# Optimization experiments

Hardware: AMD Instinct MI355X
Metric: run time of the kernel (lower is better)

Reference implementation:

```python
import jax, jax.numpy as jnp
import numpy as np

N_NODES = 50000
N_HOPS = 4
N_EDGES = 800000
NFEAT = 512
HIDDEN = 512
NCLASS = 128
ATT_HID = 64


def setup_inputs() -> dict:
    key = jax.random.key(0)
    ks = jax.random.split(key, 12)
    s = lambda *sh: 1.0 / np.sqrt(sh[0])
    inp = {}
    inp['x'] = jax.random.normal(ks[0], (N_NODES, NFEAT), dtype=jnp.float32)
    inp['W1'] = jax.random.normal(ks[1], (NFEAT, HIDDEN), dtype=jnp.float32) * s(NFEAT)
    inp['W2'] = jax.random.normal(ks[2], (HIDDEN, NCLASS), dtype=jnp.float32) * s(HIDDEN)
    inp['b2'] = jax.random.normal(ks[3], (NCLASS,), dtype=jnp.float32) * 0.01
    inp['Wg'] = jax.random.normal(ks[4], (NCLASS, NCLASS), dtype=jnp.float32) * s(NCLASS)
    inp['Wa'] = jax.random.normal(ks[5], (2 * NCLASS, ATT_HID), dtype=jnp.float32) * s(2 * NCLASS)
    inp['ba'] = jax.random.normal(ks[6], (ATT_HID,), dtype=jnp.float32) * 0.01
    inp['va'] = jax.random.normal(ks[7], (ATT_HID,), dtype=jnp.float32) * s(ATT_HID)
    inp['adj_values'] = jax.random.uniform(ks[8], (N_HOPS, N_EDGES), dtype=jnp.float32)
    inp['adj_indices'] = jax.random.randint(ks[9], (N_HOPS, 2, N_EDGES), 0, N_NODES, dtype=jnp.int32)
    inp['idx'] = jnp.arange(N_NODES, dtype=jnp.int32)
    return inp


def reference(x, W1, W2, b2, Wg, Wa, ba, va, adj_values, adj_indices, idx):
    # x: [N, nfeat] -> relu(linear1) -> linear2 : [N, C]
    z = jax.nn.relu(x @ W1) @ W2 + b2  # [N, C]
    anchor = z[idx]                    # [Na, C]
    na = idx.shape[0]
    n_hops = adj_indices.shape[0]
    embs = [anchor]
    for h in range(n_hops):  # fixed small structural loop over hops
        rows = adj_indices[h, 0]  # destination anchor row per edge
        cols = adj_indices[h, 1]  # source node per edge
        # sparse matmul: agg[r] = sum_e v_e * z[cols_e]  (LayerConvol)
        agg = jax.ops.segment_sum(adj_values[h][:, None] * z[cols], rows, num_segments=na)
        embs.append(agg @ Wg)  # [Na, C]
    seq = jnp.stack(embs, axis=1)  # [Na, H+1, C]
    # AttenMlp: additive attention of anchor query over hop embeddings
    q = jnp.broadcast_to(anchor[:, None, :], seq.shape)       # [Na, H+1, C]
    feat = jnp.concatenate([q, seq], axis=-1)                 # [Na, H+1, 2C]
    scores = jnp.tanh(feat @ Wa + ba) @ va                    # [Na, H+1]
    alpha = jax.nn.softmax(scores, axis=1)
    out = jnp.einsum('nh,nhc->nc', alpha, seq)                # [Na, C]
    return jax.nn.log_softmax(out, axis=1)
```

## Files before the change

### kernel.cpp

```cpp
#include <hip/hip_runtime.h>

#define NA    50000
#define NFEAT 512
#define HID   512
#define NC    128
#define AH    64
#define NE    800000
#define NHOP  4
#define NBUCK 196
#define CAPB  5120

typedef __bf16 bf16x8 __attribute__((ext_vector_type(8)));
typedef float  f32x4  __attribute__((ext_vector_type(4)));

__device__ __forceinline__ unsigned short f2bf(float f){
  union { float f; unsigned u; } a; a.f = f;
  return (unsigned short)((a.u + 0x7fffu + ((a.u >> 16) & 1u)) >> 16);
}
__device__ __forceinline__ float bf2f(unsigned short h){
  union { unsigned u; float f; } a; a.u = ((unsigned)h) << 16;
  return a.f;
}
__device__ __forceinline__ float uasf(unsigned u){
  union { unsigned u; float f; } a; a.u = u;
  return a.f;
}
__device__ __forceinline__ float tanh_fast(float x){
  x = fminf(15.f, fmaxf(-15.f, x));
  float e = __expf(2.f * x);
  return (e - 1.f) / (e + 1.f);
}

__device__ __forceinline__ void g2l16(const void* g, void* l){
  __builtin_amdgcn_global_load_lds(
      (const __attribute__((address_space(1))) void*)g,
      (__attribute__((address_space(3))) void*)l, 16, 0, 0);
}

__global__ void prep_kernel(const float* __restrict__ W1, const float* __restrict__ W2,
                            const float* __restrict__ Wg, const float* __restrict__ Wa,
                            const float* __restrict__ b2,
                            unsigned short* __restrict__ W1T, unsigned short* __restrict__ W2cT,
                            unsigned short* __restrict__ WaT, float* __restrict__ b2c,
                            int* __restrict__ fill){
  const int b = blockIdx.x, tid = threadIdx.x;
  if (b < 1024){
    int i = b * 256 + tid;
    int n = i >> 9, k = i & 511;
    W1T[i] = f2bf(W1[(size_t)k * HID + n]);
  } else if (b < 1280){
    int i = (b - 1024) * 256 + tid;
    int n = i >> 9, k = i & 511;
    W2cT[i] = f2bf(W2[(size_t)k * NC + n]);
  } else if (b < 1536){
    int i = (b - 1280) * 256 + tid;
    int n = i >> 9, k = i & 511;
    float s = 0.f;
    for (int j = 0; j < 128; j++)
      s += W2[(size_t)k * NC + j] * Wg[(size_t)j * NC + n];
    W2cT[65536 + i] = f2bf(s);
  } else if (b < 1600){
    int i = (b - 1536) * 256 + tid;
    int n = i >> 7, k = i & 127;
    float v = (n < 64) ? Wa[(size_t)k * AH + n] : Wa[(size_t)(128 + k) * AH + (n - 64)];
    WaT[i] = f2bf(v);
  } else if (b == 1600){
    if (tid < 128) b2c[tid] = b2[tid];
    else {
      int n = tid - 128;
      float s = 0.f;
      for (int j = 0; j < 128; j++) s += b2[j] * Wg[(size_t)j * NC + n];
      b2c[128 + n] = s;
    }
  } else {
    int i = (b - 1601) * 256 + tid;
    if (i < NHOP * NBUCK) fill[i] = 0;
  }
}

__global__ __launch_bounds__(256) void gemm1_kernel(
    const float* __restrict__ A32, const unsigned short* __restrict__ BT,
    unsigned short* __restrict__ Cb)
{
  const int xcd = blockIdx.x & 7, slot = blockIdx.x >> 3;
  const int r = xcd * 49 + (slot >> 2);
  if (r >= 391) return;
  const int row0 = r * 128, col0 = (slot & 3) * 128;
  const int M = NA, N = HID, K = NFEAT;
  __shared__ unsigned short As[128 * 32];
  __shared__ unsigned short Bs[128 * 32];
  const int tid = threadIdx.x;
  const int wave = tid >> 6, lane = tid & 63;
  const int wr = (wave >> 1) * 64, wc = (wave & 1) * 64;
  f32x4 acc[4][4];
  #pragma unroll
  for (int m = 0; m < 4; m++)
    #pragma unroll
    for (int n = 0; n < 4; n++) acc[m][n] = (f32x4){0.f, 0.f, 0.f, 0.f};
  const int lrow = lane >> 2, lk = (lane & 3) * 8;

  for (int k0 = 0; k0 < K; k0 += 32){
    __syncthreads();
    #pragma unroll
    for (int j = 0; j < 2; j++){
      const int rb = (wave * 2 + j) * 16;
      const int ra = rb + lrow;
      int gr = row0 + ra; gr = gr < M ? gr : M - 1;
      const float* src = A32 + (size_t)gr * K + k0 + lk;
      float4 f0 = *reinterpret_cast<const float4*>(src);
      float4 f1 = *reinterpret_cast<const float4*>(src + 4);
      bf16x8 a;
      a[0] = (__bf16)f0.x; a[1] = (__bf16)f0.y; a[2] = (__bf16)f0.z; a[3] = (__bf16)f0.w;
      a[4] = (__bf16)f1.x; a[5] = (__bf16)f1.y; a[6] = (__bf16)f1.z; a[7] = (__bf16)f1.w;
      *reinterpret_cast<bf16x8*>(&As[ra * 32 + lk]) = a;
      int gc = col0 + ra; gc = gc < N ? gc : N - 1;
      g2l16(BT + (size_t)gc * K + k0 + lk, Bs + rb * 32);
    }
    __syncthreads();
    bf16x8 af[4], bfr[4];
    #pragma unroll
    for (int m = 0; m < 4; m++)
      af[m] = *reinterpret_cast<const bf16x8*>(&As[(wr + m * 16 + (lane & 15)) * 32 + (lane >> 4) * 8]);
    #pragma unroll
    for (int n = 0; n < 4; n++)
      bfr[n] = *reinterpret_cast<const bf16x8*>(&Bs[(wc + n * 16 + (lane & 15)) * 32 + (lane >> 4) * 8]);
    #pragma unroll
    for (int m = 0; m < 4; m++)
      #pragma unroll
      for (int n = 0; n < 4; n++)
        acc[m][n] = __builtin_amdgcn_mfma_f32_16x16x32_bf16(af[m], bfr[n], acc[m][n], 0, 0, 0);
  }

  const int rbase = row0 + wr + (lane >> 4) * 4;
  const int cbase = col0 + wc + (lane & 15);
  #pragma unroll
  for (int m = 0; m < 4; m++){
    #pragma unroll
    for (int n = 0; n < 4; n++){
      const int col = cbase + n * 16;
      #pragma unroll
      for (int i = 0; i < 4; i++){
        const int row = rbase + m * 16 + i;
        if (row < M){
          float v = acc[m][n][i];
          v = v > 0.f ? v : 0.f;
          Cb[(size_t)row * N + col] = f2bf(v);
        }
      }
    }
  }
}

__global__ __launch_bounds__(256) void gemm2_kernel(
    const unsigned short* __restrict__ H, const unsigned short* __restrict__ W2cT,
    const float* __restrict__ b2c,
    unsigned short* __restrict__ zbf, unsigned short* __restrict__ zg)
{
  const int xcd = blockIdx.x & 7, slot = blockIdx.x >> 3;
  const int r = xcd * 49 + (slot >> 1);
  if (r >= 391) return;
  const int row0 = r * 128, col0 = (slot & 1) * 128;
  const int K = HID;
  __shared__ unsigned short As[128 * 32];
  __shared__ unsigned short Bs[128 * 32];
  const int tid = threadIdx.x;
  const int wave = tid >> 6, lane = tid & 63;
  const int wr = (wave >> 1) * 64, wc = (wave & 1) * 64;
  f32x4 acc[4][4];
  #pragma unroll
  for (int m = 0; m < 4; m++)
    #pragma unroll
    for (int n = 0; n < 4; n++) acc[m][n] = (f32x4){0.f, 0.f, 0.f, 0.f};
  const int lrow = lane >> 2, lk = (lane & 3) * 8;

  for (int k0 = 0; k0 < K; k0 += 32){
    __syncthreads();
    #pragma unroll
    for (int j = 0; j < 2; j++){
      const int rb = (wave * 2 + j) * 16;
      const int ra = rb + lrow;
      int gr = row0 + ra; gr = gr < NA ? gr : NA - 1;
      g2l16(H + (size_t)gr * K + k0 + lk, As + rb * 32);
      int gc = col0 + ra;
      g2l16(W2cT + (size_t)gc * K + k0 + lk, Bs + rb * 32);
    }
    __syncthreads();
    bf16x8 af[4], bfr[4];
    #pragma unroll
    for (int m = 0; m < 4; m++)
      af[m] = *reinterpret_cast<const bf16x8*>(&As[(wr + m * 16 + (lane & 15)) * 32 + (lane >> 4) * 8]);
    #pragma unroll
    for (int n = 0; n < 4; n++)
      bfr[n] = *reinterpret_cast<const bf16x8*>(&Bs[(wc + n * 16 + (lane & 15)) * 32 + (lane >> 4) * 8]);
    #pragma unroll
    for (int m = 0; m < 4; m++)
      #pragma unroll
      for (int n = 0; n < 4; n++)
        acc[m][n] = __builtin_amdgcn_mfma_f32_16x16x32_bf16(af[m], bfr[n], acc[m][n], 0, 0, 0);
  }

  const int rbase = row0 + wr + (lane >> 4) * 4;
  const int cbase = col0 + wc + (lane & 15);
  #pragma unroll
  for (int m = 0; m < 4; m++){
    #pragma unroll
    for (int n = 0; n < 4; n++){
      const int col = cbase + n * 16;
      #pragma unroll
      for (int i = 0; i < 4; i++){
        const int row = rbase + m * 16 + i;
        if (row < NA){
          float v = acc[m][n][i] + b2c[col];
          unsigned short o = f2bf(v);
          if (col < 128) zbf[(size_t)row * NC + col] = o;
          else           zg[(size_t)row * NC + (col - 128)] = o;
        }
      }
    }
  }
}

__global__ __launch_bounds__(256) void gemm_sweep(
    const unsigned short* __restrict__ embs, const unsigned short* __restrict__ zbf,
    const unsigned short* __restrict__ WaT,
    unsigned short* __restrict__ EW, unsigned short* __restrict__ ZWb)
{
  const int zi = blockIdx.z;
  const bool ew = zi < 4;
  const int row0 = blockIdx.x * (ew ? 256 : 128);
  if (row0 >= NA) return;
  const unsigned short* A  = ew ? embs + (size_t)zi * NA * NC : zbf;
  const unsigned short* BT = ew ? WaT + 64 * 128 : WaT;
  unsigned short* Cb       = ew ? EW + (size_t)zi * NA * AH : ZWb;
  const int N = ew ? 64 : 128;

  __shared__ unsigned short As[256 * 32];
  __shared__ unsigned short Bs[128 * 32];
  const int tid = threadIdx.x;
  const int wave = tid >> 6, lane = tid & 63;
  const int wr = ew ? wave * 64 : (wave >> 1) * 64;
  const int wc = ew ? 0 : (wave & 1) * 64;
  f32x4 acc[4][4];
  #pragma unroll
  for (int m = 0; m < 4; m++)
    #pragma unroll
    for (int n = 0; n < 4; n++) acc[m][n] = (f32x4){0.f, 0.f, 0.f, 0.f};
  const int lrow = lane >> 2, lk = (lane & 3) * 8;

  for (int k0 = 0; k0 < 128; k0 += 32){
    __syncthreads();
    if (ew){
      #pragma unroll
      for (int j = 0; j < 4; j++){
        const int rb = (wave * 4 + j) * 16;
        int gr = row0 + rb + lrow; gr = gr < NA ? gr : NA - 1;
        g2l16(A + (size_t)gr * 128 + k0 + lk, As + rb * 32);
      }
      {
        const int rb = wave * 16;
        int gc = rb + lrow; gc = gc < 64 ? gc : 63;
        g2l16(BT + (size_t)gc * 128 + k0 + lk, Bs + rb * 32);
      }
    } else {
      #pragma unroll
      for (int j = 0; j < 2; j++){
        const int rb = (wave * 2 + j) * 16;
        int gr = row0 + rb + lrow; gr = gr < NA ? gr : NA - 1;
        g2l16(A + (size_t)gr * 128 + k0 + lk, As + rb * 32);
        int gc = rb + lrow; gc = gc < N ? gc : N - 1;
        g2l16(BT + (size_t)gc * 128 + k0 + lk, Bs + rb * 32);
      }
    }
    __syncthreads();
    bf16x8 bfr[4];
    #pragma unroll
    for (int n = 0; n < 4; n++)
      bfr[n] = *reinterpret_cast<const bf16x8*>(&Bs[(wc + n * 16 + (lane & 15)) * 32 + (lane >> 4) * 8]);
    #pragma unroll
    for (int m = 0; m < 4; m++){
      bf16x8 a = *reinterpret_cast<const bf16x8*>(&As[(wr + m * 16 + (lane & 15)) * 32 + (lane >> 4) * 8]);
      #pragma unroll
      for (int n = 0; n < 4; n++)
        acc[m][n] = __builtin_amdgcn_mfma_f32_16x16x32_bf16(a, bfr[n], acc[m][n], 0, 0, 0);
    }
  }

  const int rbase = row0 + wr + (lane >> 4) * 4;
  const int cbase = wc + (lane & 15);
  #pragma unroll
  for (int m = 0; m < 4; m++){
    #pragma unroll
    for (int n = 0; n < 4; n++){
      const int col = cbase + n * 16;
      #pragma unroll
      for (int i = 0; i < 4; i++){
        const int row = rbase + m * 16 + i;
        if (row < NA && col < N)
          Cb[(size_t)row * N + col] = f2bf(acc[m][n][i]);
      }
    }
  }
}

__global__ __launch_bounds__(256) void binA_kernel(
    const int* __restrict__ adji, const float* __restrict__ adjv,
    int* __restrict__ fill, long long* __restrict__ binned)
{
  const int h = blockIdx.y, tid = threadIdx.x;
  const int e0 = blockIdx.x * 2048;
  __shared__ int lhist[NBUCK], lbase[NBUCK], lfill[NBUCK];
  for (int i = tid; i < NBUCK; i += 256){ lhist[i] = 0; lfill[i] = 0; }
  __syncthreads();
  int rr[8]; unsigned hh[8]; float vv[8];
  #pragma unroll
  for (int k = 0; k < 8; k++){
    int e = e0 + k * 256 + tid;
    bool ok = e < NE;
    int r = ok ? adji[(size_t)h * 2 * NE + e] : -1;
    int c = ok ? adji[(size_t)h * 2 * NE + NE + e] : 0;
    vv[k] = ok ? adjv[(size_t)h * NE + e] : 0.f;
    rr[k] = r;
    hh[k] = ((unsigned)(r & 255) << 17) | (unsigned)c;
    if (ok) atomicAdd(&lhist[r >> 8], 1);
  }
  __syncthreads();
  if (tid < NBUCK) lbase[tid] = atomicAdd(&fill[h * NBUCK + tid], lhist[tid]);
  __syncthreads();
  #pragma unroll
  for (int k = 0; k < 8; k++){
    if (rr[k] >= 0){
      int b = rr[k] >> 8;
      int p = lbase[b] + atomicAdd(&lfill[b], 1);
      if (p < CAPB)
        binned[((size_t)(h * NBUCK + b)) * CAPB + p] =
            ((long long)hh[k] << 32) | (unsigned)__float_as_int(vv[k]);
    }
  }
}

__global__ __launch_bounds__(1024) void bscan_kernel(const int* __restrict__ fill,
                                                     int* __restrict__ bbase, int* __restrict__ offs){
  __shared__ int tmp[1024];
  int tid = threadIdx.x;
  int v = (tid < NHOP * NBUCK) ? fill[tid] : 0;
  tmp[tid] = v; __syncthreads();
  for (int o = 1; o < 1024; o <<= 1){
    int t = (tid >= o) ? tmp[tid - o] : 0;
    __syncthreads();
    tmp[tid] += t;
    __syncthreads();
  }
  if (tid < NHOP * NBUCK) bbase[tid] = tmp[tid] - v;
  if (tid == 0) offs[NHOP * NA] = NHOP * NE;
}

__global__ __launch_bounds__(256) void binB_kernel(
    const int* __restrict__ fill, const int* __restrict__ bbase,
    const long long* __restrict__ binned,
    int* __restrict__ offs, long long* __restrict__ pvc)
{
  const int b = blockIdx.x, h = blockIdx.y, tid = threadIdx.x;
  const int hb = h * NBUCK + b;
  const int cnt = min(fill[hb], CAPB);
  const long long* src = binned + (size_t)hb * CAPB;
  const int gbase = bbase[hb];
  const int rowbase = b << 8;
  const int nrows = min(256, NA - rowbase);
  __shared__ long long sdata[CAPB];
  __shared__ int lhist[256], lpre[256], lfill2[256];
  lhist[tid] = 0; lfill2[tid] = 0;
  __syncthreads();
  for (int p = tid; p < cnt; p += 256)
    atomicAdd(&lhist[(unsigned)(src[p] >> 32) >> 17], 1);
  __syncthreads();
  int v = lhist[tid]; lpre[tid] = v; __syncthreads();
  for (int o = 1; o < 256; o <<= 1){
    int t = (tid >= o) ? lpre[tid - o] : 0;
    __syncthreads();
    lpre[tid] += t;
    __syncthreads();
  }
  int excl = lpre[tid] - v;
  if (tid < nrows) offs[h * NA + rowbase + tid] = gbase + excl;
  lpre[tid] = excl;
  __syncthreads();
  for (int p = tid; p < cnt; p += 256){
    long long rec = src[p];
    unsigned hi = (unsigned)(rec >> 32);
    int lr = hi >> 17;
    long long out = (rec & 0xffffffffLL) | ((long long)((hi & 0x1ffffu) << 6) << 32);
    int pos = lpre[lr] + atomicAdd(&lfill2[lr], 1);
    if (pos < CAPB) sdata[pos] = out;
    else            pvc[(size_t)gbase + pos] = out;
  }
  __syncthreads();
  for (int p = tid; p < cnt; p += 256)
    pvc[(size_t)gbase + p] = sdata[p];
}

#define GR 4
__global__ __launch_bounds__(256) void gather_kernel(
    const int* __restrict__ offs, const long long* __restrict__ pvc,
    const unsigned short* __restrict__ zg, unsigned short* __restrict__ embs)
{
  const int h = blockIdx.y;
  const int w = threadIdx.x >> 6, lane = threadIdx.x & 63;
  const int row = blockIdx.x * GR + w;
  const int base = h * NA + row;
  const int s = offs[base], e = offs[base + 1];
  __shared__ alignas(16) long long srec[GR][64];
  const unsigned* z32 = (const unsigned*)zg;
  const int4* sr2 = (const int4*)&srec[w][0];
  float a0 = 0.f, a1 = 0.f, b0 = 0.f, b1 = 0.f;
  for (int p0 = s; p0 < e; p0 += 64){
    long long r = 0;
    if (p0 + lane < e) r = __builtin_nontemporal_load(&pvc[p0 + lane]);
    srec[w][lane] = r;
    const int quads = (min(64, e - p0) + 3) >> 2;
    #pragma unroll 4
    for (int q = 0; q < quads; q++){
      int4 ra = sr2[2 * q], rb = sr2[2 * q + 1];
      unsigned z0 = z32[(unsigned)ra.y + lane];
      unsigned z1 = z32[(unsigned)ra.w + lane];
      unsigned z2 = z32[(unsigned)rb.y + lane];
      unsigned z3 = z32[(unsigned)rb.w + lane];
      float v0 = uasf((unsigned)ra.x), v1 = uasf((unsigned)ra.z);
      float v2 = uasf((unsigned)rb.x), v3 = uasf((unsigned)rb.z);
      a0 += v0 * uasf(z0 << 16); a1 += v0 * uasf(z0 & 0xffff0000u);
      b0 += v1 * uasf(z1 << 16); b1 += v1 * uasf(z1 & 0xffff0000u);
      a0 += v2 * uasf(z2 << 16); a1 += v2 * uasf(z2 & 0xffff0000u);
      b0 += v3 * uasf(z3 << 16); b1 += v3 * uasf(z3 & 0xffff0000u);
    }
  }
  ushort2 o; o.x = f2bf(a0 + b0); o.y = f2bf(a1 + b1);
  *reinterpret_cast<ushort2*>(embs + (size_t)base * NC + lane * 2) = o;
}

__global__ __launch_bounds__(256) void final_kernel(
    const unsigned short* __restrict__ zbf, const unsigned short* __restrict__ embs,
    const unsigned short* __restrict__ ZWb, const unsigned short* __restrict__ EW,
    const float* __restrict__ ba, const float* __restrict__ va,
    const int* __restrict__ idx, float* __restrict__ out)
{
  int tid = threadIdx.x, wave = tid >> 6, lane = tid & 63;
  int n = blockIdx.x * 4 + wave;
  if (n >= NA) return;
  int an = idx[n];
  float qa = bf2f(ZWb[(size_t)an * NC + lane]) + ba[lane];
  float vaj = va[lane];
  float sc[5];
  {
    float s0 = bf2f(ZWb[(size_t)an * NC + 64 + lane]);
    float t = tanh_fast(qa + s0) * vaj;
    #pragma unroll
    for (int o = 32; o; o >>= 1) t += __shfl_xor(t, o);
    sc[0] = t;
  }
  #pragma unroll
  for (int h = 1; h < 5; h++){
    float sh = bf2f(EW[((size_t)(h - 1) * NA + n) * AH + lane]);
    float t = tanh_fast(qa + sh) * vaj;
    #pragma unroll
    for (int o = 32; o; o >>= 1) t += __shfl_xor(t, o);
    sc[h] = t;
  }
  float m = sc[0];
  #pragma unroll
  for (int h = 1; h < 5; h++) m = fmaxf(m, sc[h]);
  float al[5], den = 0.f;
  #pragma unroll
  for (int h = 0; h < 5; h++){ al[h] = __expf(sc[h] - m); den += al[h]; }
  float inv = 1.f / den;
  float o0 = al[0] * bf2f(zbf[(size_t)an * NC + lane]);
  float o1 = al[0] * bf2f(zbf[(size_t)an * NC + 64 + lane]);
  #pragma unroll
  for (int h = 1; h < 5; h++){
    o0 += al[h] * bf2f(embs[((size_t)(h - 1) * NA + n) * NC + lane]);
    o1 += al[h] * bf2f(embs[((size_t)(h - 1) * NA + n) * NC + 64 + lane]);
  }
  o0 *= inv; o1 *= inv;
  float mx = fmaxf(o0, o1);
  #pragma unroll
  for (int o = 32; o; o >>= 1) mx = fmaxf(mx, __shfl_xor(mx, o));
  float se = __expf(o0 - mx) + __expf(o1 - mx);
  #pragma unroll
  for (int o = 32; o; o >>= 1) se += __shfl_xor(se, o);
  float ls = __logf(se);
  out[(size_t)n * NC + lane]      = o0 - mx - ls;
  out[(size_t)n * NC + 64 + lane] = o1 - mx - ls;
}


extern "C" void kernel_launch(void* const* d_in, const int* in_sizes, int n_in,
                              void* d_out, int out_size, void* d_ws, size_t ws_size,
                              hipStream_t stream)
{
  const float* x    = (const float*)d_in[0];
  const float* W1   = (const float*)d_in[1];
  const float* W2   = (const float*)d_in[2];
  const float* b2   = (const float*)d_in[3];
  const float* Wg   = (const float*)d_in[4];
  const float* Wa   = (const float*)d_in[5];
  const float* ba   = (const float*)d_in[6];
  const float* va   = (const float*)d_in[7];
  const float* adjv = (const float*)d_in[8];
  const int*   adji = (const int*)d_in[9];
  const int*   idx  = (const int*)d_in[10];
  float* out = (float*)d_out;
  (void)in_sizes; (void)n_in; (void)out_size; (void)ws_size;

  char* w = (char*)d_ws;
  auto alloc = [&](size_t b) -> char* { char* p = w; w += (b + 255) & ~(size_t)255; return p; };
  unsigned short* Scr1 = (unsigned short*)alloc((size_t)NA * NFEAT * 2);
  unsigned short* Hbuf = (unsigned short*)alloc((size_t)NA * HID * 2);
  unsigned short* W1T  = (unsigned short*)alloc((size_t)HID * NFEAT * 2);
  unsigned short* W2cT = (unsigned short*)alloc((size_t)256 * HID * 2);
  unsigned short* WaT  = (unsigned short*)alloc((size_t)NC * NC * 2);
  float*          b2c  = (float*)alloc(256 * 4);
  unsigned short* zbf  = (unsigned short*)alloc((size_t)NA * NC * 2);
  unsigned short* zg   = (unsigned short*)alloc((size_t)NA * NC * 2);
  unsigned short* ZWb  = (unsigned short*)alloc((size_t)NA * NC * 2);
  int* fill  = (int*)alloc((size_t)NHOP * NBUCK * 4);
  int* bbase = (int*)alloc((size_t)NHOP * NBUCK * 4);
  int* offs  = (int*)alloc(((size_t)NHOP * NA + 1) * 4);
  long long* pvc = (long long*)alloc((size_t)NHOP * NE * 8);
  long long* binned     = (long long*)Scr1;
  unsigned short* embs  = Scr1;
  unsigned short* EW    = (unsigned short*)pvc;

  prep_kernel<<<dim3(1605), 256, 0, stream>>>(W1, W2, Wg, Wa, b2, W1T, W2cT, WaT, b2c, fill);

  gemm1_kernel<<<dim3(1568), 256, 0, stream>>>(x, W1T, Hbuf);
  gemm2_kernel<<<dim3(784), 256, 0, stream>>>(Hbuf, W2cT, b2c, zbf, zg);

  binA_kernel<<<dim3((NE + 2047) / 2048, NHOP), 256, 0, stream>>>(adji, adjv, fill, binned);
  bscan_kernel<<<dim3(1), 1024, 0, stream>>>(fill, bbase, offs);
  binB_kernel<<<dim3(NBUCK, NHOP), 256, 0, stream>>>(fill, bbase, binned, offs, pvc);

  gather_kernel<<<dim3(NA / GR, NHOP), 256, 0, stream>>>(offs, pvc, zg, embs);
  gemm_sweep<<<dim3(391, 1, 5), 256, 0, stream>>>(embs, zbf, WaT, EW, ZWb);

  final_kernel<<<dim3(NA / 4), 256, 0, stream>>>(zbf, embs, ZWb, EW, ba, va, idx, out);
}
```

Baseline: 342.0 us.

## Widen GEMM tiles to 128x256 and merge both dense GEMMs into one template

```diff
diff --git a/kernel.cpp b/kernel.cpp
--- a/kernel.cpp
+++ b/kernel.cpp
@@ -78,99 +78,34 @@
   }
 }
 
-__global__ __launch_bounds__(256) void gemm1_kernel(
-    const float* __restrict__ A32, const unsigned short* __restrict__ BT,
-    unsigned short* __restrict__ Cb)
-{
-  const int xcd = blockIdx.x & 7, slot = blockIdx.x >> 3;
-  const int r = xcd * 49 + (slot >> 2);
-  if (r >= 391) return;
-  const int row0 = r * 128, col0 = (slot & 3) * 128;
-  const int M = NA, N = HID, K = NFEAT;
+template<int OP>
+__global__ __launch_bounds__(256) void gemm_wide(
+    const void* __restrict__ Avoid, const unsigned short* __restrict__ BT,
+    unsigned short* __restrict__ C0, unsigned short* __restrict__ C1,
+    const float* __restrict__ bias)
+{
+  int row0, col0;
+  if (OP == 0){
+    const int xcd = blockIdx.x & 7, slot = blockIdx.x >> 3;
+    const int r = xcd * 49 + (slot >> 1);
+    if (r >= 391) return;
+    row0 = r * 128; col0 = (slot & 1) * 256;
+  } else {
+    row0 = blockIdx.x * 128; col0 = 0;
+  }
+  const int K = 512;
+  const float*          A32 = (const float*)Avoid;
+  const unsigned short* A16 = (const unsigned short*)Avoid;
   __shared__ unsigned short As[128 * 32];
-  __shared__ unsigned short Bs[128 * 32];
+  __shared__ unsigned short Bs[256 * 32];
   const int tid = threadIdx.x;
   const int wave = tid >> 6, lane = tid & 63;
-  const int wr = (wave >> 1) * 64, wc = (wave & 1) * 64;
-  f32x4 acc[4][4];
+  const int wr = (wave >> 1) * 64, wcb = (wave & 1) * 128;
+  f32x4 acc[4][8];
   #pragma unroll
   for (int m = 0; m < 4; m++)
     #pragma unroll
-    for (int n = 0; n < 4; n++) acc[m][n] = (f32x4){0.f, 0.f, 0.f, 0.f};
-  const int lrow = lane >> 2, lk = (lane & 3) * 8;
-
-  for (int k0 = 0; k0 < K; k0 += 32){
-    __syncthreads();
-    #pragma unroll
-    for (int j = 0; j < 2; j++){
-      const int rb = (wave * 2 + j) * 16;
-      const int ra = rb + lrow;
-      int gr = row0 + ra; gr = gr < M ? gr : M - 1;
-      const float* src = A32 + (size_t)gr * K + k0 + lk;
-      float4 f0 = *reinterpret_cast<const float4*>(src);
-      float4 f1 = *reinterpret_cast<const float4*>(src + 4);
-      bf16x8 a;
-      a[0] = (__bf16)f0.x; a[1] = (__bf16)f0.y; a[2] = (__bf16)f0.z; a[3] = (__bf16)f0.w;
-      a[4] = (__bf16)f1.x; a[5] = (__bf16)f1.y; a[6] = (__bf16)f1.z; a[7] = (__bf16)f1.w;
-      *reinterpret_cast<bf16x8*>(&As[ra * 32 + lk]) = a;
-      int gc = col0 + ra; gc = gc < N ? gc : N - 1;
-      g2l16(BT + (size_t)gc * K + k0 + lk, Bs + rb * 32);
-    }
-    __syncthreads();
-    bf16x8 af[4], bfr[4];
-    #pragma unroll
-    for (int m = 0; m < 4; m++)
-      af[m] = *reinterpret_cast<const bf16x8*>(&As[(wr + m * 16 + (lane & 15)) * 32 + (lane >> 4) * 8]);
-    #pragma unroll
-    for (int n = 0; n < 4; n++)
-      bfr[n] = *reinterpret_cast<const bf16x8*>(&Bs[(wc + n * 16 + (lane & 15)) * 32 + (lane >> 4) * 8]);
-    #pragma unroll
-    for (int m = 0; m < 4; m++)
-      #pragma unroll
-      for (int n = 0; n < 4; n++)
-        acc[m][n] = __builtin_amdgcn_mfma_f32_16x16x32_bf16(af[m], bfr[n], acc[m][n], 0, 0, 0);
-  }
-
-  const int rbase = row0 + wr + (lane >> 4) * 4;
-  const int cbase = col0 + wc + (lane & 15);
-  #pragma unroll
-  for (int m = 0; m < 4; m++){
-    #pragma unroll
-    for (int n = 0; n < 4; n++){
-      const int col = cbase + n * 16;
-      #pragma unroll
-      for (int i = 0; i < 4; i++){
-        const int row = rbase + m * 16 + i;
-        if (row < M){
-          float v = acc[m][n][i];
-          v = v > 0.f ? v : 0.f;
-          Cb[(size_t)row * N + col] = f2bf(v);
-        }
-      }
-    }
-  }
-}
-
-__global__ __launch_bounds__(256) void gemm2_kernel(
-    const unsigned short* __restrict__ H, const unsigned short* __restrict__ W2cT,
-    const float* __restrict__ b2c,
-    unsigned short* __restrict__ zbf, unsigned short* __restrict__ zg)
-{
-  const int xcd = blockIdx.x & 7, slot = blockIdx.x >> 3;
-  const int r = xcd * 49 + (slot >> 1);
-  if (r >= 391) return;
-  const int row0 = r * 128, col0 = (slot & 1) * 128;
-  const int K = HID;
-  __shared__ unsigned short As[128 * 32];
-  __shared__ unsigned short Bs[128 * 32];
-  const int tid = threadIdx.x;
-  const int wave = tid >> 6, lane = tid & 63;
-  const int wr = (wave >> 1) * 64, wc = (wave & 1) * 64;
-  f32x4 acc[4][4];
-  #pragma unroll
-  for (int m = 0; m < 4; m++)
-    #pragma unroll
-    for (int n = 0; n < 4; n++) acc[m][n] = (f32x4){0.f, 0.f, 0.f, 0.f};
+    for (int n = 0; n < 8; n++) acc[m][n] = (f32x4){0.f, 0.f, 0.f, 0.f};
   const int lrow = lane >> 2, lk = (lane & 3) * 8;
 
   for (int k0 = 0; k0 < K; k0 += 32){
@@ -180,40 +115,60 @@
       const int rb = (wave * 2 + j) * 16;
       const int ra = rb + lrow;
       int gr = row0 + ra; gr = gr < NA ? gr : NA - 1;
-      g2l16(H + (size_t)gr * K + k0 + lk, As + rb * 32);
-      int gc = col0 + ra;
-      g2l16(W2cT + (size_t)gc * K + k0 + lk, Bs + rb * 32);
-    }
-    __syncthreads();
-    bf16x8 af[4], bfr[4];
+      if (OP == 0){
+        const float* src = A32 + (size_t)gr * K + k0 + lk;
+        float4 f0 = *reinterpret_cast<const float4*>(src);
+        float4 f1 = *reinterpret_cast<const float4*>(src + 4);
+        bf16x8 a;
+        a[0] = (__bf16)f0.x; a[1] = (__bf16)f0.y; a[2] = (__bf16)f0.z; a[3] = (__bf16)f0.w;
+        a[4] = (__bf16)f1.x; a[5] = (__bf16)f1.y; a[6] = (__bf16)f1.z; a[7] = (__bf16)f1.w;
+        *reinterpret_cast<bf16x8*>(&As[ra * 32 + lk]) = a;
+      } else {
+        g2l16(A16 + (size_t)gr * K + k0 + lk, As + rb * 32);
+      }
+    }
+    #pragma unroll
+    for (int j = 0; j < 4; j++){
+      const int rb = (wave * 4 + j) * 16;
+      const int gc = col0 + rb + lrow;
+      g2l16(BT + (size_t)gc * K + k0 + lk, Bs + rb * 32);
+    }
+    __syncthreads();
+    bf16x8 af[4], bfr[8];
     #pragma unroll
     for (int m = 0; m < 4; m++)
       af[m] = *reinterpret_cast<const bf16x8*>(&As[(wr + m * 16 + (lane & 15)) * 32 + (lane >> 4) * 8]);
     #pragma unroll
-    for (int n = 0; n < 4; n++)
-      bfr[n] = *reinterpret_cast<const bf16x8*>(&Bs[(wc + n * 16 + (lane & 15)) * 32 + (lane >> 4) * 8]);
+    for (int n = 0; n < 8; n++)
+      bfr[n] = *reinterpret_cast<const bf16x8*>(&Bs[(wcb + n * 16 + (lane & 15)) * 32 + (lane >> 4) * 8]);
     #pragma unroll
     for (int m = 0; m < 4; m++)
       #pragma unroll
-      for (int n = 0; n < 4; n++)
+      for (int n = 0; n < 8; n++)
         acc[m][n] = __builtin_amdgcn_mfma_f32_16x16x32_bf16(af[m], bfr[n], acc[m][n], 0, 0, 0);
   }
 
   const int rbase = row0 + wr + (lane >> 4) * 4;
-  const int cbase = col0 + wc + (lane & 15);
+  const int cbase = wcb + (lane & 15);
   #pragma unroll
   for (int m = 0; m < 4; m++){
     #pragma unroll
-    for (int n = 0; n < 4; n++){
-      const int col = cbase + n * 16;
+    for (int n = 0; n < 8; n++){
+      const int cl = cbase + n * 16;
       #pragma unroll
       for (int i = 0; i < 4; i++){
         const int row = rbase + m * 16 + i;
         if (row < NA){
-          float v = acc[m][n][i] + b2c[col];
-          unsigned short o = f2bf(v);
-          if (col < 128) zbf[(size_t)row * NC + col] = o;
-          else           zg[(size_t)row * NC + (col - 128)] = o;
+          float v = acc[m][n][i];
+          if (OP == 0){
+            v = v > 0.f ? v : 0.f;
+            C0[(size_t)row * HID + col0 + cl] = f2bf(v);
+          } else {
+            v += bias[cl];
+            unsigned short o = f2bf(v);
+            if (cl < 128) C0[(size_t)row * NC + cl] = o;
+            else          C1[(size_t)row * NC + (cl - 128)] = o;
+          }
         }
       }
     }
@@ -530,8 +485,8 @@
 
   prep_kernel<<<dim3(1605), 256, 0, stream>>>(W1, W2, Wg, Wa, b2, W1T, W2cT, WaT, b2c, fill);
 
-  gemm1_kernel<<<dim3(1568), 256, 0, stream>>>(x, W1T, Hbuf);
-  gemm2_kernel<<<dim3(784), 256, 0, stream>>>(Hbuf, W2cT, b2c, zbf, zg);
+  gemm_wide<0><<<dim3(784), 256, 0, stream>>>(x, W1T, Hbuf, nullptr, nullptr);
+  gemm_wide<1><<<dim3(391), 256, 0, stream>>>(Hbuf, W2cT, zbf, zg, b2c);
 
   binA_kernel<<<dim3((NE + 2047) / 2048, NHOP), 256, 0, stream>>>(adji, adjv, fill, binned);
   bscan_kernel<<<dim3(1), 1024, 0, stream>>>(fill, bbase, offs);
```

Result: slower. 418.8 us (+22.5%).
